# Optimization experiments

Measured on AMD Instinct MI355X. Metric: run time of the kernel, lower is better.

Reference implementation:

```python
import jax, jax.numpy as jnp
import numpy as np

B, A, C = 8, 19206, 91          # batch, anchors, classes (incl. background at idx 0)
K = 256                          # pre-NMS top-k candidates per class
MAX_DET = 100                    # max detections per class and final per image
IOU_T = 0.6                      # NMS IoU threshold
SCALES = (10.0, 10.0, 5.0, 5.0)


def decode_boxes(enc, anchors):
    # enc: [B,A,4] (ty,tx,th,tw); anchors: [A,4] (yc,xc,h,w) -> corners [B,A,4]
    ty = enc[..., 0] / SCALES[0]
    tx = enc[..., 1] / SCALES[1]
    th = enc[..., 2] / SCALES[2]
    tw = enc[..., 3] / SCALES[3]
    ya, xa, ha, wa = anchors[:, 0], anchors[:, 1], anchors[:, 2], anchors[:, 3]
    yc = ty * ha + ya
    xc = tx * wa + xa
    h = jnp.exp(th) * ha
    w = jnp.exp(tw) * wa
    return jnp.stack([yc - h / 2, xc - w / 2, yc + h / 2, xc + w / 2], axis=-1)


def iou_matrix(b):
    # b: [K,4] corners -> [K,K] IoU
    area = (b[:, 2] - b[:, 0]) * (b[:, 3] - b[:, 1])
    tl = jnp.maximum(b[:, None, :2], b[None, :, :2])
    br = jnp.minimum(b[:, None, 2:], b[None, :, 2:])
    wh = jnp.clip(br - tl, 0.0)
    inter = wh[..., 0] * wh[..., 1]
    union = area[:, None] + area[None, :] - inter
    return inter / jnp.maximum(union, 1e-8)


def nms_single(boxes, scores):
    # boxes [K,4], scores [K] (sigmoid scores, >0). Greedy NMS, MAX_DET picks.
    iou = iou_matrix(boxes)

    def step(s, _):
        i = jnp.argmax(s)
        val = s[i]
        keep = val > 0.0  # suppressed entries are set to -1
        s_new = jnp.where(iou[i] >= IOU_T, -1.0, s)
        return s_new, (i, jnp.where(keep, val, 0.0), keep)

    _, (idx, vals, valid) = jax.lax.scan(step, scores, None, length=MAX_DET)
    sel_boxes = boxes[idx] * valid[:, None].astype(boxes.dtype)
    return sel_boxes, vals, valid


def reference(box_encodings, class_logits, anchors):
    decoded = decode_boxes(box_encodings, anchors)            # [B,A,4]
    scores = jax.nn.sigmoid(class_logits)[..., 1:]            # drop background: [B,A,C-1]
    sc = jnp.transpose(scores, (0, 2, 1))                     # [B,C-1,A]
    top_s, top_i = jax.lax.top_k(sc, K)                       # [B,C-1,K]
    boxes_sel = jnp.take_along_axis(decoded[:, None], top_i[..., None], axis=2)  # [B,C-1,K,4]
    sel_boxes, sel_scores, _ = jax.vmap(jax.vmap(nms_single))(boxes_sel, top_s)  # [B,C-1,MAX_DET,*]
    Cc = C - 1
    cls = jnp.broadcast_to(
        jnp.arange(1, C, dtype=decoded.dtype)[None, :, None], (B, Cc, MAX_DET))
    flat_scores = sel_scores.reshape(B, -1)                   # [B,(C-1)*MAX_DET]
    flat_boxes = sel_boxes.reshape(B, -1, 4)
    flat_cls = cls.reshape(B, -1)
    fin_s, fin_i = jax.lax.top_k(flat_scores, MAX_DET)        # [B,MAX_DET]
    fin_boxes = jnp.take_along_axis(flat_boxes, fin_i[..., None], axis=1)
    fin_cls = jnp.take_along_axis(flat_cls, fin_i, axis=1)
    # detections: [boxes(4), class(1), score(1)] -> [B,MAX_DET,6]
    return jnp.concatenate([fin_boxes, fin_cls[..., None], fin_s[..., None]], axis=2)


def setup_inputs() -> dict:
    key = jax.random.key(0)
    k1, k2, k3 = jax.random.split(key, 3)
    box_encodings = jax.random.normal(k1, (B, A, 4), dtype=jnp.float32)
    class_logits = jax.random.normal(k2, (B, A, C), dtype=jnp.float32)
    anchors = jax.random.uniform(k3, (A, 4), dtype=jnp.float32)  # yc,xc,h,w in (0,1)
    return {"box_encodings": box_encodings, "class_logits": class_logits, "anchors": anchors}
```

## Files before the change

kernel.cpp:

```cpp
#include <hip/hip_runtime.h>
#include <stdint.h>
#include <math.h>

typedef unsigned int u32;
typedef unsigned long long u64;

#define BB 8
#define AA 19206
#define CCH 91
#define NCLS 90
#define KSEL 256
#define MAXDET 100
#define NROWS (BB*NCLS)
#define NFLAT (NCLS*MAXDET)
#define IOU_T 0.6f

#define ATILE 64
__global__ void __launch_bounds__(256) k_sigT(const float* __restrict__ logits,
                                              float* __restrict__ sc, int b0) {
  __shared__ __align__(16) float tile[ATILE * CCH];
  int bl = blockIdx.y;
  int b  = b0 + bl;
  int a0 = blockIdx.x * ATILE;
  int nt = AA - a0; if (nt > ATILE) nt = ATILE;
  int nload = nt * CCH;
  const float* src = logits + ((size_t)b * AA + a0) * CCH;
  const float2* s2 = (const float2*)src;
  int n2 = nload >> 1;
  for (int i = threadIdx.x; i < n2; i += 256) ((float2*)tile)[i] = s2[i];
  __syncthreads();
  for (int j = threadIdx.x; j < ATILE * NCLS; j += 256) {
    int c  = j >> 6;
    int ai = j & 63;
    if (ai < nt) {
      float x = tile[ai * CCH + (c + 1)];
      float s = 1.0f / (1.0f + expf(-x));
      sc[((size_t)bl * NCLS + c) * AA + a0 + ai] = s;
    }
  }
}

__global__ void __launch_bounds__(512) k_row(const float* __restrict__ sc,
    float* __restrict__ tks, int* __restrict__ tki, int row0) {
  __shared__ u32 hist[256];
  __shared__ u32 suf[256];
  __shared__ u64 cand[512];
  __shared__ int shBs, ctr;
  int rl  = blockIdx.x;
  int row = row0 + rl;
  int tid = threadIdx.x;
  const float2* src = (const float2*)(sc + (size_t)rl * AA);
  if (tid < 256) hist[tid] = 0;
  if (tid == 0) ctr = 0;
  __syncthreads();
  for (int i = tid; i < AA / 2; i += 512) {
    float2 v = src[i];
    atomicAdd(&hist[min(255, (int)(v.x * 256.0f))], 1u);
    atomicAdd(&hist[min(255, (int)(v.y * 256.0f))], 1u);
  }
  __syncthreads();
  if (tid < 256) suf[tid] = hist[tid];
  __syncthreads();
  for (int off = 1; off < 256; off <<= 1) {
    u32 v = 0;
    if (tid < 256 && tid + off < 256) v = suf[tid + off];
    __syncthreads();
    if (tid < 256) suf[tid] += v;
    __syncthreads();
  }
  if (tid < 256) {
    u32 nxt = (tid < 255) ? suf[tid + 1] : 0u;
    if (suf[tid] >= (u32)KSEL && nxt < (u32)KSEL) shBs = tid;
  }
  __syncthreads();
  int Bs = shBs;
  int lane = tid & 63;
  for (int i = tid; i < AA / 2; i += 512) {
    float2 v = src[i];
    {
      bool p = min(255, (int)(v.x * 256.0f)) >= Bs;
      u64 m = __ballot(p);
      if (p) {
        int leader = (int)(__ffsll((long long)m) - 1);
        int base = 0;
        if (lane == leader) base = atomicAdd(&ctr, (int)__popcll(m));
        base = __shfl(base, leader);
        int pos = base + (int)__popcll(m & ((1ull << lane) - 1ull));
        if (pos < 512)
          cand[pos] = ((u64)__float_as_uint(v.x) << 32) | (u32)(~(u32)(2 * i));
      }
    }
    {
      bool p = min(255, (int)(v.y * 256.0f)) >= Bs;
      u64 m = __ballot(p);
      if (p) {
        int leader = (int)(__ffsll((long long)m) - 1);
        int base = 0;
        if (lane == leader) base = atomicAdd(&ctr, (int)__popcll(m));
        base = __shfl(base, leader);
        int pos = base + (int)__popcll(m & ((1ull << lane) - 1ull));
        if (pos < 512)
          cand[pos] = ((u64)__float_as_uint(v.y) << 32) | (u32)(~(u32)(2 * i + 1));
      }
    }
  }
  __syncthreads();
  int n = ctr < 512 ? ctr : 512;
  for (int i = n + tid; i < 512; i += 512) cand[i] = 0;
  __syncthreads();
  for (int k = 2; k <= 512; k <<= 1) {
    for (int j = k >> 1; j > 0; j >>= 1) {
      int l = tid ^ j;
      if (l > tid) {
        u64 x = cand[tid], y = cand[l];
        bool asc = ((tid & k) == 0);
        if ((x > y) == asc) { cand[tid] = y; cand[l] = x; }
      }
      __syncthreads();
    }
  }
  if (tid < KSEL) {
    u64 kk = cand[511 - tid];
    tks[(size_t)row * KSEL + tid] = __uint_as_float((u32)(kk >> 32));
    tki[(size_t)row * KSEL + tid] = (int)(~(u32)kk);
  }
}

__device__ inline float rdlane(float x, int l) {
  return __int_as_float(__builtin_amdgcn_readlane(__float_as_int(x), l));
}

__device__ inline float4 decode1(const float* __restrict__ enc,
                                 const float* __restrict__ anch, int b, int ai) {
  float4 e  = ((const float4*)enc)[(size_t)b * AA + ai];
  float4 an = ((const float4*)anch)[ai];
  float ty = e.x / 10.0f, tx = e.y / 10.0f, th = e.z / 5.0f, tw = e.w / 5.0f;
  float yc = ty * an.z + an.x;
  float xc = tx * an.w + an.y;
  float h  = expf(th) * an.z;
  float w  = expf(tw) * an.w;
  float4 o;
  o.x = yc - h * 0.5f; o.y = xc - w * 0.5f; o.z = yc + h * 0.5f; o.w = xc + w * 0.5f;
  return o;
}

__global__ void __launch_bounds__(256) k_nms(const float* __restrict__ enc,
    const float* __restrict__ anch,
    const float* __restrict__ tks, const int* __restrict__ tki,
    float* __restrict__ flat_s, float* __restrict__ flat_b) {
  int wid = threadIdx.x >> 6, lane = threadIdx.x & 63;
  int row = blockIdx.x * 4 + wid;
  int b = row / NCLS, c = row % NCLS;
  const float* trow = tks + (size_t)row * KSEL;
  const int*   irow = tki + (size_t)row * KSEL;
  float s0 = trow[lane], s1 = trow[64 + lane], s2 = trow[128 + lane], s3 = trow[192 + lane];
  int   i0 = irow[lane], i1 = irow[64 + lane], i2 = irow[128 + lane], i3 = irow[192 + lane];
  float4 B0 = decode1(enc, anch, b, i0);
  float4 B1 = decode1(enc, anch, b, i1);
  float4 B2 = decode1(enc, anch, b, i2);
  float4 B3 = decode1(enc, anch, b, i3);
  float a0 = (B0.z - B0.x) * (B0.w - B0.y);
  float a1 = (B1.z - B1.x) * (B1.w - B1.y);
  float a2 = (B2.z - B2.x) * (B2.w - B2.y);
  float a3 = (B3.z - B3.x) * (B3.w - B3.y);
  u64 m0 = __ballot(s0 > 0.0f);
  u64 m1 = __ballot(s1 > 0.0f);
  u64 m2 = __ballot(s2 > 0.0f);
  u64 m3 = __ballot(s3 > 0.0f);
  const float cP = __uint_as_float(0x3F199999u);
  const double M = 0.5 * ((double)cP + (double)0.6f);
  float ss0 = 0.0f, ss1 = 0.0f;
  float4 ob0; ob0.x = ob0.y = ob0.z = ob0.w = 0.0f;
  float4 ob1 = ob0;
  size_t fo = (size_t)b * NFLAT + (size_t)c * MAXDET;
  for (int d = 0; d < MAXDET; d++) {
    int kw; u64 w;
    if      (m0) { kw = 0; w = m0; }
    else if (m1) { kw = 1; w = m1; }
    else if (m2) { kw = 2; w = m2; }
    else if (m3) { kw = 3; w = m3; }
    else break;
    int lw = (int)__builtin_ctzll(w);
    float sw_, wx_, wy_, wz_, ww_;
    if (kw == 0) {
      sw_ = rdlane(s0, lw);
      wx_ = rdlane(B0.x, lw); wy_ = rdlane(B0.y, lw);
      wz_ = rdlane(B0.z, lw); ww_ = rdlane(B0.w, lw);
    } else if (kw == 1) {
      sw_ = rdlane(s1, lw);
      wx_ = rdlane(B1.x, lw); wy_ = rdlane(B1.y, lw);
      wz_ = rdlane(B1.z, lw); ww_ = rdlane(B1.w, lw);
    } else if (kw == 2) {
      sw_ = rdlane(s2, lw);
      wx_ = rdlane(B2.x, lw); wy_ = rdlane(B2.y, lw);
      wz_ = rdlane(B2.z, lw); ww_ = rdlane(B2.w, lw);
    } else {
      sw_ = rdlane(s3, lw);
      wx_ = rdlane(B3.x, lw); wy_ = rdlane(B3.y, lw);
      wz_ = rdlane(B3.z, lw); ww_ = rdlane(B3.w, lw);
    }
    bool c0 = (lane == d);
    bool c1 = (lane + 64 == d);
    ss0 = c0 ? sw_ : ss0;
    ob0.x = c0 ? wx_ : ob0.x; ob0.y = c0 ? wy_ : ob0.y;
    ob0.z = c0 ? wz_ : ob0.z; ob0.w = c0 ? ww_ : ob0.w;
    ss1 = c1 ? sw_ : ss1;
    ob1.x = c1 ? wx_ : ob1.x; ob1.y = c1 ? wy_ : ob1.y;
    ob1.z = c1 ? wz_ : ob1.z; ob1.w = c1 ? ww_ : ob1.w;
    float ia = (wz_ - wx_) * (ww_ - wy_);
    float in0, in1, in2, in3, un0, un1, un2, un3;
#define PAIR(BX, AK, INK, UNK) { \
      float ty = fmaxf(wx_, BX.x), tx = fmaxf(wy_, BX.y); \
      float by = fminf(wz_, BX.z), bw = fminf(ww_, BX.w); \
      float hh = fmaxf(by - ty, 0.0f), wvv = fmaxf(bw - tx, 0.0f); \
      INK = hh * wvv; \
      UNK = fmaxf(ia + AK - INK, 1e-8f); }
    PAIR(B0, a0, in0, un0)
    PAIR(B1, a1, in1, un1)
    PAIR(B2, a2, in2, un2)
    PAIR(B3, a3, in3, un3)
#undef PAIR
    u64 cm0 = __ballot((double)in0 >= M * (double)un0);
    u64 cm1 = __ballot((double)in1 >= M * (double)un1);
    u64 cm2 = __ballot((double)in2 >= M * (double)un2);
    u64 cm3 = __ballot((double)in3 >= M * (double)un3);
    m0 &= ~cm0; m1 &= ~cm1; m2 &= ~cm2; m3 &= ~cm3;
  }
  flat_s[fo + lane] = ss0;
  ((float4*)flat_b)[fo + lane] = ob0;
  if (lane < MAXDET - 64) {
    flat_s[fo + 64 + lane] = ss1;
    ((float4*)flat_b)[fo + 64 + lane] = ob1;
  }
}

__device__ inline void bitonic_u64_asc(u64* a, int n, int tid) {
  for (int k = 2; k <= n; k <<= 1) {
    for (int j = k >> 1; j > 0; j >>= 1) {
      for (int i = tid; i < n; i += 256) {
        int l = i ^ j;
        if (l > i) {
          u64 x = a[i], y = a[l];
          bool asc = ((i & k) == 0);
          if ((x > y) == asc) { a[i] = y; a[l] = x; }
        }
      }
      __syncthreads();
    }
  }
}
__device__ inline void bitonic_u32_asc(u32* a, int n, int tid) {
  for (int k = 2; k <= n; k <<= 1) {
    for (int j = k >> 1; j > 0; j >>= 1) {
      for (int i = tid; i < n; i += 256) {
        int l = i ^ j;
        if (l > i) {
          u32 x = a[i], y = a[l];
          bool asc = ((i & k) == 0);
          if ((x > y) == asc) { a[i] = y; a[l] = x; }
        }
      }
      __syncthreads();
    }
  }
}

template<typename F>
__device__ inline void radix_select(F getv, int n, int kwant,
    u32* hist, u32* suf, int* sh2, int tid,
    u32& V_out, int& GT_out, int& r_out) {
  int r = kwant; u32 V = 0; int GT = 0;
  for (int lvl = 0; lvl < 3; lvl++) {
    int shift = (lvl == 0) ? 19 : ((lvl == 1) ? 8 : 0);
    int nbins = (lvl == 2) ? 256 : 2048;
    for (int i = tid; i < nbins; i += 256) hist[i] = 0;
    __syncthreads();
    for (int idx = tid; idx < n; idx += 256) {
      u32 u = __float_as_uint(getv(idx));
      bool ok = (lvl == 0) || (lvl == 1 ? ((u >> 19) == (V >> 19))
                                        : ((u >> 8)  == (V >> 8)));
      u64 zm = __ballot(ok && u == 0u);
      if (ok) {
        if (u == 0u) {
          if ((int)(threadIdx.x & 63) == (int)(__ffsll((long long)zm) - 1))
            atomicAdd(&hist[0], (u32)__popcll(zm));
        } else {
          atomicAdd(&hist[(u >> shift) & (u32)(nbins - 1)], 1u);
        }
      }
    }
    __syncthreads();
    int G = nbins >> 8;
    u32 ps = 0;
    for (int g = 0; g < G; g++) ps += hist[tid * G + g];
    suf[tid] = ps;
    __syncthreads();
    for (int off = 1; off < 256; off <<= 1) {
      u32 v = (tid + off < 256) ? suf[tid + off] : 0u;
      __syncthreads();
      suf[tid] += v;
      __syncthreads();
    }
    u32 sufnext = (tid < 255) ? suf[tid + 1] : 0u;
    if (suf[tid] >= (u32)r && sufnext < (u32)r) {
      u32 cum = sufnext; int kb = tid * G;
      for (int bin = tid * G + G - 1; bin >= tid * G; bin--) {
        cum += hist[bin];
        if (cum >= (u32)r) { kb = bin; break; }
      }
      sh2[0] = kb;
      sh2[1] = (int)(cum - hist[kb]);
    }
    __syncthreads();
    int kb = sh2[0], gt = sh2[1];
    r -= gt; GT += gt; V |= ((u32)kb) << shift;
    __syncthreads();
  }
  V_out = V; GT_out = GT; r_out = r;
}

__global__ void __launch_bounds__(256) k_topk_direct(const float* __restrict__ src,
    float* __restrict__ tks, int* __restrict__ tki) {
  __shared__ u32 hist[2048];
  __shared__ u32 suf[256];
  __shared__ int sh2[2];
  __shared__ u64 sel[KSEL];
  __shared__ u32 tie[512];
  __shared__ int cgt, ctie;
  int row = blockIdx.x, tid = threadIdx.x;
  int b = row / NCLS, c = row % NCLS;
  const float* base = src + (size_t)b * AA * CCH + (c + 1);
  auto getv = [&](int i) -> float {
    float x = base[(size_t)i * CCH]; return 1.0f / (1.0f + expf(-x));
  };
  u32 V; int GT, r;
  radix_select(getv, AA, KSEL, hist, suf, sh2, tid, V, GT, r);
  if (tid == 0) { cgt = 0; ctie = 0; }
  __syncthreads();
  for (int i = tid; i < AA; i += 256) {
    u32 u = __float_as_uint(getv(i));
    if (u > V) {
      int p = atomicAdd(&cgt, 1);
      sel[p] = ((u64)u << 32) | (u32)(~(u32)i);
    } else if (u == V) {
      int p = atomicAdd(&ctie, 1);
      if (p < 512) tie[p] = (u32)i;
    }
  }
  __syncthreads();
  int nt = ctie < 512 ? ctie : 512;
  for (int i = tid + nt; i < 512; i += 256) tie[i] = 0xFFFFFFFFu;
  __syncthreads();
  bitonic_u32_asc(tie, 512, tid);
  for (int i = tid; i < r; i += 256)
    sel[GT + i] = ((u64)V << 32) | (u32)(~tie[i]);
  __syncthreads();
  bitonic_u64_asc(sel, KSEL, tid);
  for (int j = tid; j < KSEL; j += 256) {
    u64 kk = sel[KSEL - 1 - j];
    tks[(size_t)row * KSEL + j] = __uint_as_float((u32)(kk >> 32));
    tki[(size_t)row * KSEL + j] = (int)(~(u32)kk);
  }
}

__global__ void __launch_bounds__(512) k_final(const float* __restrict__ flat_s,
    const float* __restrict__ flat_b, float* __restrict__ out) {
  __shared__ u32 hist[256];
  __shared__ u32 suf[256];
  __shared__ u64 cand[512];
  __shared__ int shBs, ctr;
  int b = blockIdx.x, tid = threadIdx.x;
  int lane = tid & 63;
  const float2* src = (const float2*)(flat_s + (size_t)b * NFLAT);
  if (tid < 256) hist[tid] = 0;
  if (tid == 0) ctr = 0;
  __syncthreads();
  for (int i = tid; i < NFLAT / 2; i += 512) {
    float2 v = src[i];
    atomicAdd(&hist[min(255, (int)(v.x * 256.0f))], 1u);
    atomicAdd(&hist[min(255, (int)(v.y * 256.0f))], 1u);
  }
  __syncthreads();
  if (tid < 256) suf[tid] = hist[tid];
  __syncthreads();
  for (int off = 1; off < 256; off <<= 1) {
    u32 v = 0;
    if (tid < 256 && tid + off < 256) v = suf[tid + off];
    __syncthreads();
    if (tid < 256) suf[tid] += v;
    __syncthreads();
  }
  if (tid < 256) {
    u32 nxt = (tid < 255) ? suf[tid + 1] : 0u;
    if (suf[tid] >= (u32)MAXDET && nxt < (u32)MAXDET) shBs = tid;
  }
  __syncthreads();
  int Bs = shBs;
  for (int i = tid; i < NFLAT / 2; i += 512) {
    float2 v = src[i];
    {
      bool p = min(255, (int)(v.x * 256.0f)) >= Bs;
      u64 m = __ballot(p);
      if (p) {
        int leader = (int)(__ffsll((long long)m) - 1);
        int base = 0;
        if (lane == leader) base = atomicAdd(&ctr, (int)__popcll(m));
        base = __shfl(base, leader);
        int pos = base + (int)__popcll(m & ((1ull << lane) - 1ull));
        if (pos < 512)
          cand[pos] = ((u64)__float_as_uint(v.x) << 32) | (u32)(~(u32)(2 * i));
      }
    }
    {
      bool p = min(255, (int)(v.y * 256.0f)) >= Bs;
      u64 m = __ballot(p);
      if (p) {
        int leader = (int)(__ffsll((long long)m) - 1);
        int base = 0;
        if (lane == leader) base = atomicAdd(&ctr, (int)__popcll(m));
        base = __shfl(base, leader);
        int pos = base + (int)__popcll(m & ((1ull << lane) - 1ull));
        if (pos < 512)
          cand[pos] = ((u64)__float_as_uint(v.y) << 32) | (u32)(~(u32)(2 * i + 1));
      }
    }
  }
  __syncthreads();
  int n = ctr < 512 ? ctr : 512;
  for (int i = n + tid; i < 512; i += 512) cand[i] = 0;
  __syncthreads();
  for (int k = 2; k <= 512; k <<= 1) {
    for (int j = k >> 1; j > 0; j >>= 1) {
      int l = tid ^ j;
      if (l > tid) {
        u64 x = cand[tid], y = cand[l];
        bool asc = ((tid & k) == 0);
        if ((x > y) == asc) { cand[tid] = y; cand[l] = x; }
      }
      __syncthreads();
    }
  }
  if (tid < MAXDET) {
    u64 kk = cand[511 - tid];
    u32 u  = (u32)(kk >> 32);
    int fi = (int)(~(u32)kk);
    float4 bb = ((const float4*)flat_b)[(size_t)b * NFLAT + fi];
    float* o = out + ((size_t)b * MAXDET + tid) * 6;
    o[0] = bb.x; o[1] = bb.y; o[2] = bb.z; o[3] = bb.w;
    o[4] = (float)(fi / 100 + 1);
    o[5] = __uint_as_float(u);
  }
}

extern "C" void kernel_launch(void* const* d_in, const int* in_sizes, int n_in,
                              void* d_out, int out_size, void* d_ws, size_t ws_size,
                              hipStream_t stream) {
  const float* enc    = (const float*)d_in[0];
  const float* logits = (const float*)d_in[1];
  const float* anch   = (const float*)d_in[2];
  float* out = (float*)d_out;
  char* ws = (char*)d_ws;

  size_t off = 0;
  auto alloc = [&](size_t bytes) {
    size_t o = off;
    off += (bytes + 255) & ~(size_t)255;
    return o;
  };
  size_t o_tks  = alloc((size_t)NROWS * KSEL * 4);
  size_t o_tki  = alloc((size_t)NROWS * KSEL * 4);
  size_t o_fls  = alloc((size_t)BB * NFLAT * 4);
  size_t o_flb  = alloc((size_t)BB * NFLAT * 16);
  size_t need_base = off;
  size_t o_sc = off;
  size_t per_batch_sc = ((size_t)NCLS * AA * 4 + 255) & ~(size_t)255;

  int CB = 0;
  for (int cb = BB; cb >= 1; cb >>= 1) {
    if (ws_size >= need_base + (size_t)cb * per_batch_sc) { CB = cb; break; }
  }

  float* tks = (float*)(ws + o_tks);
  int*   tki = (int*)  (ws + o_tki);
  float* fls = (float*)(ws + o_fls);
  float* flb = (float*)(ws + o_flb);
  float* scp = (float*)(ws + o_sc);

  if (CB > 0) {
    for (int b0 = 0; b0 < BB; b0 += CB) {
      hipLaunchKernelGGL(k_sigT, dim3((AA + ATILE - 1) / ATILE, CB), dim3(256), 0,
                         stream, logits, scp, b0);
      hipLaunchKernelGGL(k_row, dim3(NCLS * CB), dim3(512), 0, stream,
                         scp, tks, tki, b0 * NCLS);
    }
  } else {
    hipLaunchKernelGGL(k_topk_direct, dim3(NROWS), dim3(256), 0, stream,
                       logits, tks, tki);
  }
  hipLaunchKernelGGL(k_nms, dim3(NROWS / 4), dim3(256), 0, stream,
                     enc, anch, tks, tki, fls, flb);
  hipLaunchKernelGGL(k_final, dim3(BB), dim3(512), 0, stream,
                     fls, flb, out);
}
```

Baseline: 112.3 us.

## Process four NMS rows per wave with interleaved branchless greedy steps

Each wavefront now runs greedy NMS for four class rows at once, interleaving their per-step work so the independent lane reads, IoU math and ballots can hide each other's latency. The winner selection becomes branchless using selects instead of divergent if-chains, and the loop exits only once all four rows are exhausted. This cuts the grid to a quarter as many blocks and raises register pressure considerably, which lowers occupancy and leaves fewer waves to spread across CUs.

```diff
diff --git a/kernel.cpp b/kernel.cpp
--- a/kernel.cpp
+++ b/kernel.cpp
@@ -14,6 +14,7 @@
 #define NROWS (BB*NCLS)
 #define NFLAT (NCLS*MAXDET)
 #define IOU_T 0.6f
+#define RPW 4
 
 #define ATILE 64
 __global__ void __launch_bounds__(256) k_sigT(const float* __restrict__ logits,
@@ -149,88 +150,101 @@
     const float* __restrict__ tks, const int* __restrict__ tki,
     float* __restrict__ flat_s, float* __restrict__ flat_b) {
   int wid = threadIdx.x >> 6, lane = threadIdx.x & 63;
-  int row = blockIdx.x * 4 + wid;
-  int b = row / NCLS, c = row % NCLS;
-  const float* trow = tks + (size_t)row * KSEL;
-  const int*   irow = tki + (size_t)row * KSEL;
-  float s0 = trow[lane], s1 = trow[64 + lane], s2 = trow[128 + lane], s3 = trow[192 + lane];
-  int   i0 = irow[lane], i1 = irow[64 + lane], i2 = irow[128 + lane], i3 = irow[192 + lane];
-  float4 B0 = decode1(enc, anch, b, i0);
-  float4 B1 = decode1(enc, anch, b, i1);
-  float4 B2 = decode1(enc, anch, b, i2);
-  float4 B3 = decode1(enc, anch, b, i3);
-  float a0 = (B0.z - B0.x) * (B0.w - B0.y);
-  float a1 = (B1.z - B1.x) * (B1.w - B1.y);
-  float a2 = (B2.z - B2.x) * (B2.w - B2.y);
-  float a3 = (B3.z - B3.x) * (B3.w - B3.y);
-  u64 m0 = __ballot(s0 > 0.0f);
-  u64 m1 = __ballot(s1 > 0.0f);
-  u64 m2 = __ballot(s2 > 0.0f);
-  u64 m3 = __ballot(s3 > 0.0f);
+  int wave = blockIdx.x * 4 + wid;
+  float  s[RPW][4];
+  float4 B[RPW][4];
+  float  ar[RPW][4];
+  u64    m0[RPW], m1[RPW], m2[RPW], m3[RPW];
+  float  os0[RPW], os1[RPW];
+  float4 ob0[RPW], ob1[RPW];
+#pragma unroll
+  for (int r = 0; r < RPW; r++) {
+    int row = wave * RPW + r;
+    int b = row / NCLS;
+    const float* trow = tks + (size_t)row * KSEL;
+    const int*   irow = tki + (size_t)row * KSEL;
+#pragma unroll
+    for (int k = 0; k < 4; k++) {
+      s[r][k] = trow[64 * k + lane];
+      int ai  = irow[64 * k + lane];
+      B[r][k] = decode1(enc, anch, b, ai);
+      ar[r][k] = (B[r][k].z - B[r][k].x) * (B[r][k].w - B[r][k].y);
+    }
+    m0[r] = __ballot(s[r][0] > 0.0f);
+    m1[r] = __ballot(s[r][1] > 0.0f);
+    m2[r] = __ballot(s[r][2] > 0.0f);
+    m3[r] = __ballot(s[r][3] > 0.0f);
+    os0[r] = 0.0f; os1[r] = 0.0f;
+    ob0[r].x = ob0[r].y = ob0[r].z = ob0[r].w = 0.0f;
+    ob1[r] = ob0[r];
+  }
   const float cP = __uint_as_float(0x3F199999u);
   const double M = 0.5 * ((double)cP + (double)0.6f);
-  float ss0 = 0.0f, ss1 = 0.0f;
-  float4 ob0; ob0.x = ob0.y = ob0.z = ob0.w = 0.0f;
-  float4 ob1 = ob0;
-  size_t fo = (size_t)b * NFLAT + (size_t)c * MAXDET;
   for (int d = 0; d < MAXDET; d++) {
-    int kw; u64 w;
-    if      (m0) { kw = 0; w = m0; }
-    else if (m1) { kw = 1; w = m1; }
-    else if (m2) { kw = 2; w = m2; }
-    else if (m3) { kw = 3; w = m3; }
-    else break;
-    int lw = (int)__builtin_ctzll(w);
-    float sw_, wx_, wy_, wz_, ww_;
-    if (kw == 0) {
-      sw_ = rdlane(s0, lw);
-      wx_ = rdlane(B0.x, lw); wy_ = rdlane(B0.y, lw);
-      wz_ = rdlane(B0.z, lw); ww_ = rdlane(B0.w, lw);
-    } else if (kw == 1) {
-      sw_ = rdlane(s1, lw);
-      wx_ = rdlane(B1.x, lw); wy_ = rdlane(B1.y, lw);
-      wz_ = rdlane(B1.z, lw); ww_ = rdlane(B1.w, lw);
-    } else if (kw == 2) {
-      sw_ = rdlane(s2, lw);
-      wx_ = rdlane(B2.x, lw); wy_ = rdlane(B2.y, lw);
-      wz_ = rdlane(B2.z, lw); ww_ = rdlane(B2.w, lw);
-    } else {
-      sw_ = rdlane(s3, lw);
-      wx_ = rdlane(B3.x, lw); wy_ = rdlane(B3.y, lw);
-      wz_ = rdlane(B3.z, lw); ww_ = rdlane(B3.w, lw);
-    }
-    bool c0 = (lane == d);
-    bool c1 = (lane + 64 == d);
-    ss0 = c0 ? sw_ : ss0;
-    ob0.x = c0 ? wx_ : ob0.x; ob0.y = c0 ? wy_ : ob0.y;
-    ob0.z = c0 ? wz_ : ob0.z; ob0.w = c0 ? ww_ : ob0.w;
-    ss1 = c1 ? sw_ : ss1;
-    ob1.x = c1 ? wx_ : ob1.x; ob1.y = c1 ? wy_ : ob1.y;
-    ob1.z = c1 ? wz_ : ob1.z; ob1.w = c1 ? ww_ : ob1.w;
-    float ia = (wz_ - wx_) * (ww_ - wy_);
-    float in0, in1, in2, in3, un0, un1, un2, un3;
-#define PAIR(BX, AK, INK, UNK) { \
-      float ty = fmaxf(wx_, BX.x), tx = fmaxf(wy_, BX.y); \
-      float by = fminf(wz_, BX.z), bw = fminf(ww_, BX.w); \
-      float hh = fmaxf(by - ty, 0.0f), wvv = fmaxf(bw - tx, 0.0f); \
-      INK = hh * wvv; \
-      UNK = fmaxf(ia + AK - INK, 1e-8f); }
-    PAIR(B0, a0, in0, un0)
-    PAIR(B1, a1, in1, un1)
-    PAIR(B2, a2, in2, un2)
-    PAIR(B3, a3, in3, un3)
+    u64 anyw = 0;
+#pragma unroll
+    for (int r = 0; r < RPW; r++) {
+      u64 x0 = m0[r], x1 = m1[r], x2 = m2[r], x3 = m3[r];
+      u64 wa = x0 ? x0 : x1; int ba = x0 ? 0 : 64;
+      u64 wb = x2 ? x2 : x3; int bb2 = x2 ? 128 : 192;
+      bool hi = (x0 | x1) != 0;
+      u64 w = hi ? wa : wb;
+      int base = hi ? ba : bb2;
+      bool alive = (w != 0);
+      u64 wsafe = alive ? w : 1ull;
+      int pw = base + (int)__builtin_ctzll(wsafe);
+      int kk = pw >> 6, lw = pw & 63;
+      float cs = (kk == 0) ? s[r][0] : (kk == 1) ? s[r][1] : (kk == 2) ? s[r][2] : s[r][3];
+      float cx = (kk == 0) ? B[r][0].x : (kk == 1) ? B[r][1].x : (kk == 2) ? B[r][2].x : B[r][3].x;
+      float cy = (kk == 0) ? B[r][0].y : (kk == 1) ? B[r][1].y : (kk == 2) ? B[r][2].y : B[r][3].y;
+      float cz = (kk == 0) ? B[r][0].z : (kk == 1) ? B[r][1].z : (kk == 2) ? B[r][2].z : B[r][3].z;
+      float cw = (kk == 0) ? B[r][0].w : (kk == 1) ? B[r][1].w : (kk == 2) ? B[r][2].w : B[r][3].w;
+      float sw_ = rdlane(cs, lw);
+      float wx_ = rdlane(cx, lw);
+      float wy_ = rdlane(cy, lw);
+      float wz_ = rdlane(cz, lw);
+      float ww_ = rdlane(cw, lw);
+      bool c0 = alive && (lane == d);
+      bool c1 = alive && (lane + 64 == d);
+      os0[r] = c0 ? sw_ : os0[r];
+      ob0[r].x = c0 ? wx_ : ob0[r].x; ob0[r].y = c0 ? wy_ : ob0[r].y;
+      ob0[r].z = c0 ? wz_ : ob0[r].z; ob0[r].w = c0 ? ww_ : ob0[r].w;
+      os1[r] = c1 ? sw_ : os1[r];
+      ob1[r].x = c1 ? wx_ : ob1[r].x; ob1[r].y = c1 ? wy_ : ob1[r].y;
+      ob1[r].z = c1 ? wz_ : ob1[r].z; ob1[r].w = c1 ? ww_ : ob1[r].w;
+      float ia = (wz_ - wx_) * (ww_ - wy_);
+      float in0, in1, in2, in3, un0, un1, un2, un3;
+#define PAIR(K, INK, UNK) { \
+        float ty = fmaxf(wx_, B[r][K].x), tx = fmaxf(wy_, B[r][K].y); \
+        float by = fminf(wz_, B[r][K].z), bw = fminf(ww_, B[r][K].w); \
+        float hh = fmaxf(by - ty, 0.0f), wvv = fmaxf(bw - tx, 0.0f); \
+        INK = hh * wvv; \
+        UNK = fmaxf(ia + ar[r][K] - INK, 1e-8f); }
+      PAIR(0, in0, un0)
+      PAIR(1, in1, un1)
+      PAIR(2, in2, un2)
+      PAIR(3, in3, un3)
 #undef PAIR
-    u64 cm0 = __ballot((double)in0 >= M * (double)un0);
-    u64 cm1 = __ballot((double)in1 >= M * (double)un1);
-    u64 cm2 = __ballot((double)in2 >= M * (double)un2);
-    u64 cm3 = __ballot((double)in3 >= M * (double)un3);
-    m0 &= ~cm0; m1 &= ~cm1; m2 &= ~cm2; m3 &= ~cm3;
-  }
-  flat_s[fo + lane] = ss0;
-  ((float4*)flat_b)[fo + lane] = ob0;
-  if (lane < MAXDET - 64) {
-    flat_s[fo + 64 + lane] = ss1;
-    ((float4*)flat_b)[fo + 64 + lane] = ob1;
+      u64 cm0 = __ballot((double)in0 >= M * (double)un0);
+      u64 cm1 = __ballot((double)in1 >= M * (double)un1);
+      u64 cm2 = __ballot((double)in2 >= M * (double)un2);
+      u64 cm3 = __ballot((double)in3 >= M * (double)un3);
+      m0[r] &= ~cm0; m1[r] &= ~cm1; m2[r] &= ~cm2; m3[r] &= ~cm3;
+      anyw |= w;
+    }
+    if (!anyw) break;
+  }
+#pragma unroll
+  for (int r = 0; r < RPW; r++) {
+    int row = wave * RPW + r;
+    int b = row / NCLS, c = row % NCLS;
+    size_t fo = (size_t)b * NFLAT + (size_t)c * MAXDET;
+    flat_s[fo + lane] = os0[r];
+    ((float4*)flat_b)[fo + lane] = ob0[r];
+    if (lane < MAXDET - 64) {
+      flat_s[fo + 64 + lane] = os1[r];
+      ((float4*)flat_b)[fo + 64 + lane] = ob1[r];
+    }
   }
 }
 
@@ -497,7 +511,7 @@
     hipLaunchKernelGGL(k_topk_direct, dim3(NROWS), dim3(256), 0, stream,
                        logits, tks, tki);
   }
-  hipLaunchKernelGGL(k_nms, dim3(NROWS / 4), dim3(256), 0, stream,
+  hipLaunchKernelGGL(k_nms, dim3(NROWS / (4 * RPW)), dim3(256), 0, stream,
                      enc, anch, tks, tki, fls, flb);
   hipLaunchKernelGGL(k_final, dim3(BB), dim3(512), 0, stream,
                      fls, flb, out);
```

After: 239.6 us. +113.4%, slower.

## Fuse per-row score histogram into sigmoid-transpose kernel with global atomics

Applied to the files above, without the earlier changes.

The threshold histogram is now built inside the sigmoid/transpose kernel, using per-block shared-memory histograms flushed to a global per-row histogram with atomics. A small kernel derives the bin threshold and the top-k row kernel only does the candidate-gather pass, so it no longer reads each score row a second time for the histogram. Bins drop from 256 to 64, which can produce more candidates than 512 slots. That overflow would truncate the candidates and risks wrong top-k results. It also adds a memset, an extra launch and global atomic traffic.

```diff
diff --git a/kernel.cpp b/kernel.cpp
--- a/kernel.cpp
+++ b/kernel.cpp
@@ -14,11 +14,13 @@
 #define NROWS (BB*NCLS)
 #define NFLAT (NCLS*MAXDET)
 #define IOU_T 0.6f
+#define NBIN 64
 
 #define ATILE 64
 __global__ void __launch_bounds__(256) k_sigT(const float* __restrict__ logits,
-                                              float* __restrict__ sc, int b0) {
+    float* __restrict__ sc, u32* __restrict__ ghist, int b0) {
   __shared__ __align__(16) float tile[ATILE * CCH];
+  __shared__ u32 lhist[NCLS * 65];
   int bl = blockIdx.y;
   int b  = b0 + bl;
   int a0 = blockIdx.x * ATILE;
@@ -27,6 +29,7 @@
   const float* src = logits + ((size_t)b * AA + a0) * CCH;
   const float2* s2 = (const float2*)src;
   int n2 = nload >> 1;
+  for (int i = threadIdx.x; i < NCLS * 65; i += 256) lhist[i] = 0;
   for (int i = threadIdx.x; i < n2; i += 256) ((float2*)tile)[i] = s2[i];
   __syncthreads();
   for (int j = threadIdx.x; j < ATILE * NCLS; j += 256) {
@@ -36,49 +39,49 @@
       float x = tile[ai * CCH + (c + 1)];
       float s = 1.0f / (1.0f + expf(-x));
       sc[((size_t)bl * NCLS + c) * AA + a0 + ai] = s;
-    }
-  }
+      atomicAdd(&lhist[c * 65 + min(63, (int)(s * 64.0f))], 1u);
+    }
+  }
+  __syncthreads();
+  int rowbase = b * NCLS;
+  for (int i = threadIdx.x; i < NCLS * NBIN; i += 256) {
+    int c = i >> 6, bin = i & 63;
+    u32 v = lhist[c * 65 + bin];
+    if (v) atomicAdd(&ghist[(size_t)(rowbase + c) * NBIN + bin], v);
+  }
+}
+
+__global__ void __launch_bounds__(64) k_thresh(const u32* __restrict__ ghist,
+                                               int* __restrict__ gBs, int row0) {
+  int row = row0 + blockIdx.x;
+  int lane = threadIdx.x;
+  u32 suf = ghist[(size_t)row * NBIN + lane];
+  for (int off = 1; off < 64; off <<= 1) {
+    u32 v = __shfl_down(suf, off);
+    suf += (lane + off < 64) ? v : 0u;
+  }
+  u32 nxt = __shfl_down(suf, 1);
+  if (lane == 63) nxt = 0u;
+  if (suf >= (u32)KSEL && nxt < (u32)KSEL) gBs[row] = lane;
 }
 
 __global__ void __launch_bounds__(512) k_row(const float* __restrict__ sc,
+    const int* __restrict__ gBs,
     float* __restrict__ tks, int* __restrict__ tki, int row0) {
-  __shared__ u32 hist[256];
-  __shared__ u32 suf[256];
   __shared__ u64 cand[512];
-  __shared__ int shBs, ctr;
+  __shared__ int ctr;
   int rl  = blockIdx.x;
   int row = row0 + rl;
   int tid = threadIdx.x;
   const float2* src = (const float2*)(sc + (size_t)rl * AA);
-  if (tid < 256) hist[tid] = 0;
   if (tid == 0) ctr = 0;
-  __syncthreads();
-  for (int i = tid; i < AA / 2; i += 512) {
-    float2 v = src[i];
-    atomicAdd(&hist[min(255, (int)(v.x * 256.0f))], 1u);
-    atomicAdd(&hist[min(255, (int)(v.y * 256.0f))], 1u);
-  }
-  __syncthreads();
-  if (tid < 256) suf[tid] = hist[tid];
-  __syncthreads();
-  for (int off = 1; off < 256; off <<= 1) {
-    u32 v = 0;
-    if (tid < 256 && tid + off < 256) v = suf[tid + off];
-    __syncthreads();
-    if (tid < 256) suf[tid] += v;
-    __syncthreads();
-  }
-  if (tid < 256) {
-    u32 nxt = (tid < 255) ? suf[tid + 1] : 0u;
-    if (suf[tid] >= (u32)KSEL && nxt < (u32)KSEL) shBs = tid;
-  }
-  __syncthreads();
-  int Bs = shBs;
+  int Bs = gBs[row];
+  __syncthreads();
   int lane = tid & 63;
   for (int i = tid; i < AA / 2; i += 512) {
     float2 v = src[i];
     {
-      bool p = min(255, (int)(v.x * 256.0f)) >= Bs;
+      bool p = min(63, (int)(v.x * 64.0f)) >= Bs;
       u64 m = __ballot(p);
       if (p) {
         int leader = (int)(__ffsll((long long)m) - 1);
@@ -91,7 +94,7 @@
       }
     }
     {
-      bool p = min(255, (int)(v.y * 256.0f)) >= Bs;
+      bool p = min(63, (int)(v.y * 64.0f)) >= Bs;
       u64 m = __ballot(p);
       if (p) {
         int leader = (int)(__ffsll((long long)m) - 1);
@@ -471,6 +474,8 @@
   size_t o_tki  = alloc((size_t)NROWS * KSEL * 4);
   size_t o_fls  = alloc((size_t)BB * NFLAT * 4);
   size_t o_flb  = alloc((size_t)BB * NFLAT * 16);
+  size_t o_gh   = alloc((size_t)NROWS * NBIN * 4);
+  size_t o_gbs  = alloc((size_t)NROWS * 4);
   size_t need_base = off;
   size_t o_sc = off;
   size_t per_batch_sc = ((size_t)NCLS * AA * 4 + 255) & ~(size_t)255;
@@ -484,14 +489,19 @@
   int*   tki = (int*)  (ws + o_tki);
   float* fls = (float*)(ws + o_fls);
   float* flb = (float*)(ws + o_flb);
+  u32*   gh  = (u32*)  (ws + o_gh);
+  int*   gbs = (int*)  (ws + o_gbs);
   float* scp = (float*)(ws + o_sc);
 
   if (CB > 0) {
+    hipMemsetAsync(gh, 0, (size_t)NROWS * NBIN * 4, stream);
     for (int b0 = 0; b0 < BB; b0 += CB) {
       hipLaunchKernelGGL(k_sigT, dim3((AA + ATILE - 1) / ATILE, CB), dim3(256), 0,
-                         stream, logits, scp, b0);
+                         stream, logits, scp, gh, b0);
+      hipLaunchKernelGGL(k_thresh, dim3(NCLS * CB), dim3(64), 0, stream,
+                         gh, gbs, b0 * NCLS);
       hipLaunchKernelGGL(k_row, dim3(NCLS * CB), dim3(512), 0, stream,
-                         scp, tks, tki, b0 * NCLS);
+                         scp, gbs, tks, tki, b0 * NCLS);
     }
   } else {
     hipLaunchKernelGGL(k_topk_direct, dim3(NROWS), dim3(256), 0, stream,
```

New measurement: 155.3 us. 38.3% more time.
